# Kernel tuning notes

Hardware: AMD Instinct MI355X
Metric: run time of the kernel (lower is better)

The kernel has to match this reference:

```python
import jax, jax.numpy as jnp
import numpy as np

HIDDEN_DIM = 64
MEMORY_SLOTS = 8
SEQ_LEN = 24
VOCAB_SIZE = 64
B = 262144


def setup_inputs() -> dict:
    key = jax.random.key(0)
    ks = jax.random.split(key, 7)
    return {
        "seqs": jax.random.randint(ks[0], (B, SEQ_LEN), 0, VOCAB_SIZE, dtype=jnp.int64) if jax.config.jax_enable_x64 else jax.random.randint(ks[0], (B, SEQ_LEN), 0, VOCAB_SIZE, dtype=jnp.int32),
        "query_tok": jax.random.randint(ks[1], (B,), 0, VOCAB_SIZE, dtype=jnp.int32),
        "embed_W": jax.random.normal(ks[2], (VOCAB_SIZE + 2, HIDDEN_DIM), dtype=jnp.float32),
        "W1": jax.random.normal(ks[3], (HIDDEN_DIM, 2 * HIDDEN_DIM), dtype=jnp.float32) * 0.08,
        "b1": jax.random.normal(ks[4], (HIDDEN_DIM,), dtype=jnp.float32) * 0.02,
        "W2": jax.random.normal(ks[5], (VOCAB_SIZE, HIDDEN_DIM), dtype=jnp.float32) * 0.12,
        "b2": jax.random.normal(ks[6], (VOCAB_SIZE,), dtype=jnp.float32) * 0.02,
    }


def reference(seqs, query_tok, embed_W, W1, b1, W2, b2):
    # FIFO of size MEMORY_SLOTS over tokens t in [0, SEQ_LEN-1):
    # mem_summary depends only on the last MEMORY_SLOTS of those tokens.
    mem_toks = seqs[:, SEQ_LEN - 1 - MEMORY_SLOTS : SEQ_LEN - 1]      # [B, M]
    mem_summary = jnp.mean(embed_W[mem_toks], axis=1)                 # [B, H]
    q_emb = embed_W[query_tok]                                        # [B, H]
    x = jnp.concatenate([q_emb, mem_summary], axis=-1)               # [B, 2H]
    h = jax.nn.relu(x @ W1.T + b1)                                    # [B, H]
    logits = h @ W2.T + b2                                            # [B, V]
    return logits
```

## Files before the change

kernel.cpp:

```cpp
#include <hip/hip_runtime.h>


#define RSTRIDE_W 36
#define T2_OFF_W  (64 * RSTRIDE_W)
#define LDS_DW    (2 * 64 * RSTRIDE_W)

typedef __attribute__((ext_vector_type(4))) float    f32x4;
typedef __attribute__((ext_vector_type(4))) int      i32x4;
typedef __attribute__((ext_vector_type(8))) _Float16 f16x8;

__global__ void prep_kernel(const float* __restrict__ embed,
                            const float* __restrict__ W1,
                            const float* __restrict__ b1,
                            unsigned short* __restrict__ T) {
  const int job  = blockIdx.x * 4 + (threadIdx.x >> 6);
  const int j    = threadIdx.x & 63;
  const int t    = job & 63;
  const int half = job >> 6;
  const f32x4* w4 = (const f32x4*)(W1 + j * 128 + half * 64);
  const f32x4* e4 = (const f32x4*)(embed + t * 64);
  float acc = 0.f;
#pragma unroll
  for (int k = 0; k < 16; ++k) {
    f32x4 a = w4[k], b = e4[k];
    acc += a[0] * b[0] + a[1] * b[1] + a[2] * b[2] + a[3] * b[3];
  }
  const float outv = half ? acc * 0.125f : acc + b1[j];
  ((_Float16*)T)[half * (64 * 2 * RSTRIDE_W) + t * (2 * RSTRIDE_W) + j] =
      (_Float16)outv;
}

__global__ __launch_bounds__(256, 4) void lru_kernel(
    const int*      __restrict__ seqs,
    const int*      __restrict__ qtok,
    const float*    __restrict__ W2,
    const float*    __restrict__ b2,
    const unsigned* __restrict__ T,
    float*          __restrict__ out) {
  __shared__ __align__(16) unsigned lds[LDS_DW];
  const int tid = threadIdx.x;

  {
    const uint4* src = (const uint4*)T;
    uint4*       dst = (uint4*)lds;
#pragma unroll
    for (int r = 0; r < 4; ++r) dst[tid + r * 256] = src[tid + r * 256];
    if (tid < 128) dst[tid + 1024] = src[tid + 1024];
  }

  const int lane = tid & 63;
  const int wv   = tid >> 6;
  const int qd   = lane >> 4;
  const int l15  = lane & 15;

  f16x8 afW[4][2];
  f32x4 bb4[4];
#pragma unroll
  for (int nt = 0; nt < 4; ++nt) {
    const float* wr = W2 + (nt * 16 + l15) * 64 + qd * 8;
#pragma unroll
    for (int ks = 0; ks < 2; ++ks) {
      f32x4 w0 = *(const f32x4*)(wr + ks * 32);
      f32x4 w1 = *(const f32x4*)(wr + ks * 32 + 4);
      f16x8 f;
      f[0] = (_Float16)w0[0]; f[1] = (_Float16)w0[1];
      f[2] = (_Float16)w0[2]; f[3] = (_Float16)w0[3];
      f[4] = (_Float16)w1[0]; f[5] = (_Float16)w1[1];
      f[6] = (_Float16)w1[2]; f[7] = (_Float16)w1[3];
      afW[nt][ks] = f;
    }
    bb4[nt] = *(const f32x4*)(b2 + nt * 16 + qd * 4);
  }

  const int wbase  = blockIdx.x * 256 + wv * 64;
  const int myelem = wbase + lane;
  const int* srow  = seqs + myelem * 24;
  const i32x4 t0 = __builtin_nontemporal_load((const i32x4*)(srow + 12));
  const i32x4 t1 = __builtin_nontemporal_load((const i32x4*)(srow + 16));
  const i32x4 t2 = __builtin_nontemporal_load((const i32x4*)(srow + 20));
  const int   tq = __builtin_nontemporal_load(qtok + myelem);
  const int pk0 = t0.w | (t1.x << 8) | (t1.y << 16) | (t1.z << 24);
  const int pk1 = t1.w | (t2.x << 8) | (t2.y << 16) | (t2.z << 24);
  __syncthreads();

#pragma unroll
  for (int it = 0; it < 4; ++it) {
    const int b0  = wbase + it * 16;
    const int src = it * 16 + l15;

    const int u0 = __shfl(pk0, src);
    const int u1 = __shfl(pk1, src);
    const int qt = __shfl(tq,  src);

    f16x8 a0, a1;
    {
      const f16x8* r1 = (const f16x8*)(lds + qt * RSTRIDE_W + qd * 4);
      a0 = r1[0];
      a1 = r1[4];
    }
#pragma unroll
    for (int s = 0; s < 4; ++s) {
      const int tk = (u0 >> (8 * s)) & 63;
      const f16x8* r2 =
          (const f16x8*)(lds + T2_OFF_W + tk * RSTRIDE_W + qd * 4);
      a0 += r2[0];
      a1 += r2[4];
    }
#pragma unroll
    for (int s = 0; s < 4; ++s) {
      const int tk = (u1 >> (8 * s)) & 63;
      const f16x8* r2 =
          (const f16x8*)(lds + T2_OFF_W + tk * RSTRIDE_W + qd * 4);
      a0 += r2[0];
      a1 += r2[4];
    }
    const f16x8 z = {(_Float16)0, (_Float16)0, (_Float16)0, (_Float16)0,
                     (_Float16)0, (_Float16)0, (_Float16)0, (_Float16)0};
    const f16x8 afA = __builtin_elementwise_max(a0, z);
    const f16x8 afB = __builtin_elementwise_max(a1, z);

    float* op = out + (size_t)(b0 + l15) * 64 + qd * 4;
#pragma unroll
    for (int nt = 0; nt < 4; ++nt) {
      f32x4 a = bb4[nt];
      a = __builtin_amdgcn_mfma_f32_16x16x32_f16(afW[nt][0], afA, a, 0, 0, 0);
      a = __builtin_amdgcn_mfma_f32_16x16x32_f16(afW[nt][1], afB, a, 0, 0, 0);
      __builtin_nontemporal_store(a, (f32x4*)(op + nt * 16));
    }
  }
}

extern "C" void kernel_launch(void* const* d_in, const int* in_sizes, int n_in,
                              void* d_out, int out_size, void* d_ws, size_t ws_size,
                              hipStream_t stream) {
  const int*   seqs  = (const int*)d_in[0];
  const int*   qtokp = (const int*)d_in[1];
  const float* embed = (const float*)d_in[2];
  const float* W1    = (const float*)d_in[3];
  const float* b1    = (const float*)d_in[4];
  const float* W2    = (const float*)d_in[5];
  const float* b2    = (const float*)d_in[6];
  float*       outp  = (float*)d_out;

  prep_kernel<<<dim3(32), dim3(256), 0, stream>>>(embed, W1, b1,
                                                  (unsigned short*)d_ws);
  lru_kernel<<<dim3(1024), dim3(256), 0, stream>>>(seqs, qtokp, W2, b2,
                                                   (const unsigned*)d_ws, outp);
}
```

Measured before the change: 117.4 us.

## Fuse embedding-W1 table precompute into main kernel via per-block MFMA

Removes the separate prep kernel and has every block recompute the embed·W1 projection tables directly into LDS using f16 MFMA, with each wave handling 16 tokens for both halves. This eliminates a kernel launch, its serialization and the global round trip of the table. In exchange each of the 1024 blocks redoes the small GEMM, rereads W1 and embed from L2, and the table is now computed in f16 MFMA rather than fp32 FMA, which slightly changes precision.

Result: slower. 128.7 us (+9.7%).

```diff
diff --git a/kernel.cpp b/kernel.cpp
--- a/kernel.cpp
+++ b/kernel.cpp
@@ -2,6 +2,7 @@
 
 
 #define RSTRIDE_W 36
+#define RSTRIDE_H 72
 #define T2_OFF_W  (64 * RSTRIDE_W)
 #define LDS_DW    (2 * 64 * RSTRIDE_W)
 
@@ -9,68 +10,32 @@
 typedef __attribute__((ext_vector_type(4))) int      i32x4;
 typedef __attribute__((ext_vector_type(8))) _Float16 f16x8;
 
-__global__ void prep_kernel(const float* __restrict__ embed,
-                            const float* __restrict__ W1,
-                            const float* __restrict__ b1,
-                            unsigned short* __restrict__ T) {
-  const int job  = blockIdx.x * 4 + (threadIdx.x >> 6);
-  const int j    = threadIdx.x & 63;
-  const int t    = job & 63;
-  const int half = job >> 6;
-  const f32x4* w4 = (const f32x4*)(W1 + j * 128 + half * 64);
-  const f32x4* e4 = (const f32x4*)(embed + t * 64);
-  float acc = 0.f;
-#pragma unroll
-  for (int k = 0; k < 16; ++k) {
-    f32x4 a = w4[k], b = e4[k];
-    acc += a[0] * b[0] + a[1] * b[1] + a[2] * b[2] + a[3] * b[3];
-  }
-  const float outv = half ? acc * 0.125f : acc + b1[j];
-  ((_Float16*)T)[half * (64 * 2 * RSTRIDE_W) + t * (2 * RSTRIDE_W) + j] =
-      (_Float16)outv;
+__device__ __forceinline__ f16x8 cvt8(const float* p) {
+  f32x4 w0 = *(const f32x4*)p;
+  f32x4 w1 = *(const f32x4*)(p + 4);
+  f16x8 f;
+  f[0] = (_Float16)w0[0]; f[1] = (_Float16)w0[1];
+  f[2] = (_Float16)w0[2]; f[3] = (_Float16)w0[3];
+  f[4] = (_Float16)w1[0]; f[5] = (_Float16)w1[1];
+  f[6] = (_Float16)w1[2]; f[7] = (_Float16)w1[3];
+  return f;
 }
 
 __global__ __launch_bounds__(256, 4) void lru_kernel(
-    const int*      __restrict__ seqs,
-    const int*      __restrict__ qtok,
-    const float*    __restrict__ W2,
-    const float*    __restrict__ b2,
-    const unsigned* __restrict__ T,
-    float*          __restrict__ out) {
+    const int*   __restrict__ seqs,
+    const int*   __restrict__ qtok,
+    const float* __restrict__ embed,
+    const float* __restrict__ W1,
+    const float* __restrict__ b1,
+    const float* __restrict__ W2,
+    const float* __restrict__ b2,
+    float*       __restrict__ out) {
   __shared__ __align__(16) unsigned lds[LDS_DW];
-  const int tid = threadIdx.x;
-
-  {
-    const uint4* src = (const uint4*)T;
-    uint4*       dst = (uint4*)lds;
-#pragma unroll
-    for (int r = 0; r < 4; ++r) dst[tid + r * 256] = src[tid + r * 256];
-    if (tid < 128) dst[tid + 1024] = src[tid + 1024];
-  }
-
+  const int tid  = threadIdx.x;
   const int lane = tid & 63;
   const int wv   = tid >> 6;
   const int qd   = lane >> 4;
   const int l15  = lane & 15;
-
-  f16x8 afW[4][2];
-  f32x4 bb4[4];
-#pragma unroll
-  for (int nt = 0; nt < 4; ++nt) {
-    const float* wr = W2 + (nt * 16 + l15) * 64 + qd * 8;
-#pragma unroll
-    for (int ks = 0; ks < 2; ++ks) {
-      f32x4 w0 = *(const f32x4*)(wr + ks * 32);
-      f32x4 w1 = *(const f32x4*)(wr + ks * 32 + 4);
-      f16x8 f;
-      f[0] = (_Float16)w0[0]; f[1] = (_Float16)w0[1];
-      f[2] = (_Float16)w0[2]; f[3] = (_Float16)w0[3];
-      f[4] = (_Float16)w1[0]; f[5] = (_Float16)w1[1];
-      f[6] = (_Float16)w1[2]; f[7] = (_Float16)w1[3];
-      afW[nt][ks] = f;
-    }
-    bb4[nt] = *(const f32x4*)(b2 + nt * 16 + qd * 4);
-  }
 
   const int wbase  = blockIdx.x * 256 + wv * 64;
   const int myelem = wbase + lane;
@@ -79,6 +44,45 @@
   const i32x4 t1 = __builtin_nontemporal_load((const i32x4*)(srow + 16));
   const i32x4 t2 = __builtin_nontemporal_load((const i32x4*)(srow + 20));
   const int   tq = __builtin_nontemporal_load(qtok + myelem);
+
+  {
+    const int tbase = wv * 16;
+    const float* er = embed + (tbase + l15) * 64 + qd * 8;
+    const f16x8 ea0 = cvt8(er);
+    const f16x8 ea1 = cvt8(er + 32);
+#pragma unroll
+    for (int h = 0; h < 2; ++h) {
+#pragma unroll
+      for (int nt = 0; nt < 4; ++nt) {
+        const float* wr = W1 + (nt * 16 + l15) * 128 + h * 64 + qd * 8;
+        const f16x8 wb0 = cvt8(wr);
+        const f16x8 wb1 = cvt8(wr + 32);
+        const float binit = h ? 0.f : b1[nt * 16 + l15];
+        f32x4 a;
+        a[0] = binit; a[1] = binit; a[2] = binit; a[3] = binit;
+        a = __builtin_amdgcn_mfma_f32_16x16x32_f16(ea0, wb0, a, 0, 0, 0);
+        a = __builtin_amdgcn_mfma_f32_16x16x32_f16(ea1, wb1, a, 0, 0, 0);
+        _Float16* trow =
+            (_Float16*)lds + (size_t)(h * 64 + tbase + qd * 4) * RSTRIDE_H +
+            nt * 16 + l15;
+#pragma unroll
+        for (int r = 0; r < 4; ++r)
+          trow[(size_t)r * RSTRIDE_H] =
+              (_Float16)(h ? a[r] * 0.125f : a[r]);
+      }
+    }
+  }
+
+  f16x8 afW[4][2];
+  f32x4 bb4[4];
+#pragma unroll
+  for (int nt = 0; nt < 4; ++nt) {
+    const float* wr = W2 + (nt * 16 + l15) * 64 + qd * 8;
+    afW[nt][0] = cvt8(wr);
+    afW[nt][1] = cvt8(wr + 32);
+    bb4[nt] = *(const f32x4*)(b2 + nt * 16 + qd * 4);
+  }
+
   const int pk0 = t0.w | (t1.x << 8) | (t1.y << 16) | (t1.z << 24);
   const int pk1 = t1.w | (t2.x << 8) | (t2.y << 16) | (t2.z << 24);
   __syncthreads();
@@ -142,8 +146,8 @@
   const float* b2    = (const float*)d_in[6];
   float*       outp  = (float*)d_out;
 
-  prep_kernel<<<dim3(32), dim3(256), 0, stream>>>(embed, W1, b1,
-                                                  (unsigned short*)d_ws);
-  lru_kernel<<<dim3(1024), dim3(256), 0, stream>>>(seqs, qtokp, W2, b2,
-                                                   (const unsigned*)d_ws, outp);
+  (void)d_ws; (void)ws_size;
+
+  lru_kernel<<<dim3(1024), dim3(256), 0, stream>>>(seqs, qtokp, embed, W1, b1,
+                                                   W2, b2, outp);
 }
```
